# Optimization experiments

Hardware: AMD Instinct MI355X
Metric: run time of the kernel (lower is better)

Reference implementation:

```python
import jax, jax.numpy as jnp
import numpy as np

N_NODES = 100000
N_EDGES = 1600000
N_GRAPHS = 64
IN_CH, HID_CH, OUT_CH, N_CLS = 128, 128, 64, 2


def setup_inputs() -> dict:
    key = jax.random.key(0)
    ks = jax.random.split(key, 8)
    x = jax.random.normal(ks[0], (N_NODES, IN_CH), dtype=jnp.float32)
    edge_index = jax.random.randint(ks[1], (2, N_EDGES), 0, N_NODES)
    batch = jnp.sort(jax.random.randint(ks[2], (N_NODES,), 0, N_GRAPHS))
    glorot = lambda k, shp: jax.random.normal(k, shp, dtype=jnp.float32) / np.float32(np.sqrt(shp[0]))
    return {
        "x": x, "edge_index": edge_index, "batch": batch,
        "W1": glorot(ks[3], (IN_CH, HID_CH)), "b1": jnp.zeros((HID_CH,), jnp.float32),
        "W2": glorot(ks[4], (HID_CH, HID_CH)), "b2": jnp.zeros((HID_CH,), jnp.float32),
        "W3": glorot(ks[5], (HID_CH, OUT_CH)), "b3": jnp.zeros((OUT_CH,), jnp.float32),
        "Wfc": glorot(ks[6], (OUT_CH, N_CLS)), "bfc": jnp.zeros((N_CLS,), jnp.float32),
    }


def gcn_conv(x, src, dst, W, b):
    """PyG GCNConv: add self-loops, D^{-1/2} (A+I) D^{-1/2} (x W) + b."""
    n = x.shape[0]
    h = x @ W  # [N, out]
    # degree with self-loops: 1 + in-degree at dst
    deg = jnp.ones((n,), h.dtype).at[dst].add(1.0)
    dinv = jax.lax.rsqrt(deg)  # deg >= 1 always (self-loop)
    norm = dinv[src] * dinv[dst]  # [E]
    agg = jnp.zeros_like(h).at[dst].add(h[src] * norm[:, None])
    agg = agg + h * (dinv * dinv)[:, None]  # self-loop messages
    return agg + b


def global_mean_pool(x, batch, num_graphs):
    s = jax.ops.segment_sum(x, batch, num_segments=num_graphs)
    cnt = jax.ops.segment_sum(jnp.ones((x.shape[0],), x.dtype), batch, num_segments=num_graphs)
    return s / jnp.maximum(cnt, 1.0)[:, None]


def reference(x, edge_index, batch, W1, b1, W2, b2, W3, b3, Wfc, bfc):
    src, dst = edge_index[0], edge_index[1]
    h = jax.nn.relu(gcn_conv(x, src, dst, W1, b1))   # dropout p=0.0 (eval) -> identity
    h = jax.nn.relu(gcn_conv(h, src, dst, W2, b2))
    h = gcn_conv(h, src, dst, W3, b3)
    g = global_mean_pool(h, batch, N_GRAPHS)          # [G, OUT_CH]
    return g @ Wfc + bfc                              # [G, N_CLS]
```

## Files before the change

### kernel.cpp

```cpp
#include <hip/hip_runtime.h>
#include <hip/hip_bf16.h>


#define THREADS 256
#define BSHIFT 9
#define BSIZE 512

typedef __attribute__((ext_vector_type(8))) short short8;
typedef __attribute__((ext_vector_type(16))) float floatx16;

__device__ __forceinline__ unsigned f2bf(float f) {
    unsigned u = __float_as_uint(f);
    return (u + 0x7fffu + ((u >> 16) & 1u)) >> 16;
}

__device__ __forceinline__ void bf8_acc(uint4 v, float* ac) {
    ac[0] += __uint_as_float(v.x << 16);
    ac[1] += __uint_as_float(v.x & 0xffff0000u);
    ac[2] += __uint_as_float(v.y << 16);
    ac[3] += __uint_as_float(v.y & 0xffff0000u);
    ac[4] += __uint_as_float(v.z << 16);
    ac[5] += __uint_as_float(v.z & 0xffff0000u);
    ac[6] += __uint_as_float(v.w << 16);
    ac[7] += __uint_as_float(v.w & 0xffff0000u);
}


__global__ __launch_bounds__(THREADS) void bucket_count(const int* __restrict__ dst,
                                                        int* __restrict__ btotal,
                                                        int E, int nbuck) {
    __shared__ int cnt[BSIZE];
    for (int i = threadIdx.x; i < nbuck; i += THREADS) cnt[i] = 0;
    __syncthreads();
    for (int e = blockIdx.x * THREADS + threadIdx.x; e < E; e += gridDim.x * THREADS)
        atomicAdd(&cnt[dst[e] >> BSHIFT], 1);
    __syncthreads();
    for (int i = threadIdx.x; i < nbuck; i += THREADS) {
        int c = cnt[i];
        if (c) atomicAdd(&btotal[i], c);
    }
}

__global__ __launch_bounds__(512) void bucket_scan(const int* __restrict__ btotal,
                                                   int* __restrict__ bbase,
                                                   int* __restrict__ bcursor,
                                                   float* __restrict__ gsum,
                                                   float* __restrict__ zrow,
                                                   int nbuck, int E) {
    __shared__ int lds[512];
    int t = threadIdx.x;
    for (int i = t; i < 64 * 64; i += 512) gsum[i] = 0.0f;
    if (t < 64) zrow[t] = 0.0f;
    int v = (t < nbuck) ? btotal[t] : 0;
    lds[t] = v;
    __syncthreads();
    for (int off = 1; off < 512; off <<= 1) {
        int tv = (t >= off) ? lds[t - off] : 0;
        __syncthreads();
        lds[t] += tv;
        __syncthreads();
    }
    if (t < nbuck) {
        int excl = lds[t] - v;
        bbase[t] = excl;
        bcursor[t] = excl;
    }
    if (t == 0) bbase[nbuck] = E;
}

__global__ __launch_bounds__(THREADS) void bucket_scatter(const int* __restrict__ src,
                                                          const int* __restrict__ dst,
                                                          int* __restrict__ bcursor,
                                                          int* __restrict__ pairs, int E) {
    __shared__ int cnt[BSIZE];
    __shared__ int base[BSIZE];
    for (int i = threadIdx.x; i < BSIZE; i += THREADS) cnt[i] = 0;
    __syncthreads();
    int e0 = blockIdx.x * 2048;
    int myb[8], myrank[8], mypk[8];
#pragma unroll
    for (int j = 0; j < 8; ++j) {
        int e = e0 + j * THREADS + threadIdx.x;
        myb[j] = -1;
        if (e < E) {
            int d = dst[e];
            mypk[j] = (src[e] << BSHIFT) | (d & (BSIZE - 1));
            myb[j] = d >> BSHIFT;
            myrank[j] = atomicAdd(&cnt[myb[j]], 1);
        }
    }
    __syncthreads();
    for (int i = threadIdx.x; i < BSIZE; i += THREADS) {
        int c = cnt[i];
        base[i] = c ? atomicAdd(&bcursor[i], c) : 0;
    }
    __syncthreads();
#pragma unroll
    for (int j = 0; j < 8; ++j)
        if (myb[j] >= 0) pairs[(size_t)base[myb[j]] + myrank[j]] = mypk[j];
}

__global__ __launch_bounds__(512) void bucket_fill(const int* __restrict__ pairs,
                                                   const int* __restrict__ bbase,
                                                   int* __restrict__ row_start,
                                                   float* __restrict__ dinv,
                                                   int* __restrict__ esrc,
                                                   int N, int E, int nbuck) {
    __shared__ int cnt[BSIZE];
    __shared__ int scn[BSIZE];
    int b = blockIdx.x, t = threadIdx.x;
    int s = bbase[b], e = bbase[b + 1];
    cnt[t] = 0;
    __syncthreads();
    for (int i = s + t; i < e; i += 512) atomicAdd(&cnt[pairs[i] & (BSIZE - 1)], 1);
    __syncthreads();
    int v = cnt[t];
    scn[t] = v;
    __syncthreads();
    for (int off = 1; off < 512; off <<= 1) {
        int tv = (t >= off) ? scn[t - off] : 0;
        __syncthreads();
        scn[t] += tv;
        __syncthreads();
    }
    int excl = scn[t] - v;
    int g = (b << BSHIFT) + t;
    if (g < N) {
        row_start[g] = s + excl;
        dinv[g] = rsqrtf(1.0f + (float)v);
    }
    if (b == nbuck - 1 && t == 0) row_start[N] = E;
    scn[t] = excl;
    __syncthreads();
    for (int i = s + t; i < e; i += 512) {
        int p = pairs[i];
        int r = atomicAdd(&scn[p & (BSIZE - 1)], 1);
        esrc[s + r] = ((unsigned)p) >> BSHIFT;
    }
}

__device__ __forceinline__ void wt_pack(const float* W, uint4* Wtp, int C, int li) {
    int c = li >> 4, ch = li & 15;
    unsigned r[8];
#pragma unroll
    for (int j = 0; j < 8; ++j) r[j] = f2bf(W[(size_t)(ch * 8 + j) * C + c]);
    uint4 o;
    o.x = r[0] | (r[1] << 16);
    o.y = r[2] | (r[3] << 16);
    o.z = r[4] | (r[5] << 16);
    o.w = r[6] | (r[7] << 16);
    Wtp[li] = o;
}

__global__ __launch_bounds__(THREADS) void prep_wt_all(const float* __restrict__ W1,
                                                       const float* __restrict__ W2,
                                                       const float* __restrict__ W3,
                                                       uint4* __restrict__ Wt1,
                                                       uint4* __restrict__ Wt2,
                                                       uint4* __restrict__ Wt3) {
    int idx = blockIdx.x * THREADS + threadIdx.x;
    if (idx < 2048) wt_pack(W1, Wt1, 128, idx);
    else if (idx < 4096) wt_pack(W2, Wt2, 128, idx - 2048);
    else if (idx < 5120) wt_pack(W3, Wt3, 64, idx - 4096);
}

__global__ __launch_bounds__(THREADS) void prep_x(const float* __restrict__ x,
                                                  const float* __restrict__ dinv,
                                                  uint4* __restrict__ Z, int n) {
    int idx = blockIdx.x * THREADS + threadIdx.x;
    if (idx >= n * 16) return;
    int r = idx >> 4, c = idx & 15;
    float dv = dinv[r];
    const float* p = x + (size_t)r * 128 + c * 8;
    float4 a = *(const float4*)p;
    float4 b = *(const float4*)(p + 4);
    uint4 o;
    o.x = f2bf(a.x * dv) | (f2bf(a.y * dv) << 16);
    o.y = f2bf(a.z * dv) | (f2bf(a.w * dv) << 16);
    o.z = f2bf(b.x * dv) | (f2bf(b.y * dv) << 16);
    o.w = f2bf(b.z * dv) | (f2bf(b.w * dv) << 16);
    Z[idx] = o;
}

__global__ __launch_bounds__(THREADS) void fused_layer(const uint4* __restrict__ Z,
                                                       const uint4* __restrict__ Wt,
                                                       const int* __restrict__ row_start,
                                                       const int* __restrict__ esrc,
                                                       const float* __restrict__ dinv,
                                                       const float* __restrict__ bias,
                                                       const uint4* __restrict__ zrow,
                                                       uint4* __restrict__ out,
                                                       const uint4* __restrict__ WtP,
                                                       uint4* __restrict__ outP, int n) {
    __shared__ __align__(16) uint4 ldsX[64 * 16];
    int row0 = blockIdx.x * 64;
    int maxr = n - row0;
    if (maxr > 64) maxr = 64;
    int tid = threadIdx.x;
    int lane = tid & 15, grp = tid >> 4;
    const uint4* zl = zrow + lane;

    for (int round = 0; round < 4; ++round) {
        int r = round * 16 + grp;
        int node = row0 + r;
        int nd = (node < n) ? node : (n - 1);
        float ac[8] = {0, 0, 0, 0, 0, 0, 0, 0};
        bf8_acc(Z[(size_t)nd * 16 + lane], ac);
        float dv = dinv[nd];
        int s = row_start[nd], e = row_start[nd + 1];
        int i = s;
        int nmain = (e - s) >> 3;
        if (nmain > 0) {
            int s0 = esrc[i], s1 = esrc[i + 1], s2 = esrc[i + 2], s3 = esrc[i + 3];
            int s4 = esrc[i + 4], s5 = esrc[i + 5], s6 = esrc[i + 6], s7 = esrc[i + 7];
            for (int m = 0; m < nmain; ++m) {
                uint4 v0 = Z[(size_t)s0 * 16 + lane];
                uint4 v1 = Z[(size_t)s1 * 16 + lane];
                uint4 v2 = Z[(size_t)s2 * 16 + lane];
                uint4 v3 = Z[(size_t)s3 * 16 + lane];
                uint4 v4 = Z[(size_t)s4 * 16 + lane];
                uint4 v5 = Z[(size_t)s5 * 16 + lane];
                uint4 v6 = Z[(size_t)s6 * 16 + lane];
                uint4 v7 = Z[(size_t)s7 * 16 + lane];
                int ni = i + 8;
                int t0 = esrc[ni], t1 = esrc[ni + 1], t2 = esrc[ni + 2], t3 = esrc[ni + 3];
                int t4 = esrc[ni + 4], t5 = esrc[ni + 5], t6 = esrc[ni + 6], t7 = esrc[ni + 7];
                bf8_acc(v0, ac); bf8_acc(v1, ac); bf8_acc(v2, ac); bf8_acc(v3, ac);
                bf8_acc(v4, ac); bf8_acc(v5, ac); bf8_acc(v6, ac); bf8_acc(v7, ac);
                s0 = t0; s1 = t1; s2 = t2; s3 = t3;
                s4 = t4; s5 = t5; s6 = t6; s7 = t7;
                i = ni;
            }
        }
        if (i < e) {
            const uint4* p0 = (i + 0 < e) ? (Z + ((size_t)esrc[i + 0] * 16 + lane)) : zl;
            const uint4* p1 = (i + 1 < e) ? (Z + ((size_t)esrc[i + 1] * 16 + lane)) : zl;
            const uint4* p2 = (i + 2 < e) ? (Z + ((size_t)esrc[i + 2] * 16 + lane)) : zl;
            const uint4* p3 = (i + 3 < e) ? (Z + ((size_t)esrc[i + 3] * 16 + lane)) : zl;
            const uint4* p4 = (i + 4 < e) ? (Z + ((size_t)esrc[i + 4] * 16 + lane)) : zl;
            const uint4* p5 = (i + 5 < e) ? (Z + ((size_t)esrc[i + 5] * 16 + lane)) : zl;
            const uint4* p6 = (i + 6 < e) ? (Z + ((size_t)esrc[i + 6] * 16 + lane)) : zl;
            const uint4* p7 = (i + 7 < e) ? (Z + ((size_t)esrc[i + 7] * 16 + lane)) : zl;
            uint4 v0 = *p0; uint4 v1 = *p1; uint4 v2 = *p2; uint4 v3 = *p3;
            uint4 v4 = *p4; uint4 v5 = *p5; uint4 v6 = *p6; uint4 v7 = *p7;
            bf8_acc(v0, ac); bf8_acc(v1, ac); bf8_acc(v2, ac); bf8_acc(v3, ac);
            bf8_acc(v4, ac); bf8_acc(v5, ac); bf8_acc(v6, ac); bf8_acc(v7, ac);
        }
        uint4 o;
        o.x = f2bf(ac[0] * dv) | (f2bf(ac[1] * dv) << 16);
        o.y = f2bf(ac[2] * dv) | (f2bf(ac[3] * dv) << 16);
        o.z = f2bf(ac[4] * dv) | (f2bf(ac[5] * dv) << 16);
        o.w = f2bf(ac[6] * dv) | (f2bf(ac[7] * dv) << 16);
        ldsX[r * 16 + (lane ^ (r & 7))] = o;
    }
    __syncthreads();

    int l = tid & 63, wv = tid >> 6;
    int l31 = l & 31, half = l >> 5;
    int nt = wv & 1, mt0 = (wv >> 1) * 2;
    floatx16 acc[2];
#pragma unroll
    for (int t = 0; t < 2; ++t)
#pragma unroll
        for (int q = 0; q < 16; ++q) acc[t][q] = 0.0f;
    int xrow = nt * 32 + l31, xsw = xrow & 7;
#pragma unroll
    for (int kt = 0; kt < 8; ++kt) {
        int chunk = kt * 2 + half;
        short8 xf = *(const short8*)&ldsX[xrow * 16 + (chunk ^ xsw)];
#pragma unroll
        for (int t = 0; t < 2; ++t) {
            int c = (mt0 + t) * 32 + l31;
            short8 wf = *(const short8*)&Wt[c * 16 + chunk];
            acc[t] = __builtin_amdgcn_mfma_f32_32x32x16_bf16(wf, xf, acc[t], 0, 0, 0);
        }
    }
    __syncthreads();

    int node = nt * 32 + l31;
    float dv = (node < maxr) ? dinv[row0 + node] : 0.0f;
    char* outb = (char*)ldsX;
#pragma unroll
    for (int t = 0; t < 2; ++t) {
        int cb = (mt0 + t) * 32;
#pragma unroll
        for (int q = 0; q < 4; ++q) {
            float v[4];
#pragma unroll
            for (int m = 0; m < 4; ++m) {
                int ch = cb + 8 * q + 4 * half + m;
                float x_ = acc[t][q * 4 + m] + bias[ch];
                x_ = fmaxf(x_, 0.0f);
                v[m] = x_ * dv;
            }
            uint2 pk = make_uint2(f2bf(v[0]) | (f2bf(v[1]) << 16),
                                  f2bf(v[2]) | (f2bf(v[3]) << 16));
            int chunk = (cb >> 3) + q;
            *(uint2*)(outb + node * 256 + ((chunk ^ (node & 7)) * 16) + half * 8) = pk;
        }
    }
    __syncthreads();
    for (int idx = tid; idx < maxr * 16; idx += THREADS) {
        int r = idx >> 4, c = idx & 15;
        out[(size_t)(row0 + r) * 16 + c] = *(uint4*)(outb + r * 256 + ((c ^ (r & 7)) * 16));
    }

    if (outP) {
        floatx16 accp;
#pragma unroll
        for (int q = 0; q < 16; ++q) accp[q] = 0.0f;
        int mt = wv >> 1;
#pragma unroll
        for (int kt = 0; kt < 8; ++kt) {
            int chunk = kt * 2 + half;
            short8 xf = *(const short8*)&ldsX[xrow * 16 + (chunk ^ xsw)];
            int c = mt * 32 + l31;
            short8 wf = *(const short8*)&WtP[c * 16 + chunk];
            accp = __builtin_amdgcn_mfma_f32_32x32x16_bf16(wf, xf, accp, 0, 0, 0);
        }
        __syncthreads();
        int cb = mt * 32;
#pragma unroll
        for (int q = 0; q < 4; ++q) {
            uint2 pk = make_uint2(f2bf(accp[q * 4 + 0]) | (f2bf(accp[q * 4 + 1]) << 16),
                                  f2bf(accp[q * 4 + 2]) | (f2bf(accp[q * 4 + 3]) << 16));
            int chunk = (cb >> 3) + q;
            *(uint2*)(outb + node * 128 + ((chunk ^ (node & 7)) * 16) + half * 8) = pk;
        }
        __syncthreads();
        for (int idx = tid; idx < maxr * 8; idx += THREADS) {
            int r = idx >> 3, c = idx & 7;
            outP[(size_t)(row0 + r) * 8 + c] = *(uint4*)(outb + r * 128 + ((c ^ (r & 7)) * 16));
        }
    }
}

__global__ __launch_bounds__(THREADS) void agg_pool(const uint4* __restrict__ Ps,
                                                    const int* __restrict__ row_start,
                                                    const int* __restrict__ esrc,
                                                    const float* __restrict__ dinv,
                                                    const float* __restrict__ bias,
                                                    const int* __restrict__ batch,
                                                    const uint4* __restrict__ zrow,
                                                    float* __restrict__ gsum, int n) {
    __shared__ float gpart[32][65];
    __shared__ int used[32];
    int tid = threadIdx.x;
    int lane = tid & 7, grp = tid >> 3;
    int node = blockIdx.x * 32 + grp;
    if (tid < 32) used[tid] = 0;
    for (int idx = tid; idx < 2048; idx += THREADS) gpart[idx >> 6][idx & 63] = 0.0f;
    __syncthreads();
    int gmin = batch[blockIdx.x * 32];
    const uint4* zl = zrow + lane;
    if (node < n) {
        float ac[8] = {0, 0, 0, 0, 0, 0, 0, 0};
        bf8_acc(Ps[(size_t)node * 8 + lane], ac);
        float dv = dinv[node];
        int s = row_start[node], e = row_start[node + 1];
        int i = s;
        int nmain = (e - s) >> 3;
        if (nmain > 0) {
            int s0 = esrc[i], s1 = esrc[i + 1], s2 = esrc[i + 2], s3 = esrc[i + 3];
            int s4 = esrc[i + 4], s5 = esrc[i + 5], s6 = esrc[i + 6], s7 = esrc[i + 7];
            for (int m = 0; m < nmain; ++m) {
                uint4 v0 = Ps[(size_t)s0 * 8 + lane];
                uint4 v1 = Ps[(size_t)s1 * 8 + lane];
                uint4 v2 = Ps[(size_t)s2 * 8 + lane];
                uint4 v3 = Ps[(size_t)s3 * 8 + lane];
                uint4 v4 = Ps[(size_t)s4 * 8 + lane];
                uint4 v5 = Ps[(size_t)s5 * 8 + lane];
                uint4 v6 = Ps[(size_t)s6 * 8 + lane];
                uint4 v7 = Ps[(size_t)s7 * 8 + lane];
                int ni = i + 8;
                int t0 = esrc[ni], t1 = esrc[ni + 1], t2 = esrc[ni + 2], t3 = esrc[ni + 3];
                int t4 = esrc[ni + 4], t5 = esrc[ni + 5], t6 = esrc[ni + 6], t7 = esrc[ni + 7];
                bf8_acc(v0, ac); bf8_acc(v1, ac); bf8_acc(v2, ac); bf8_acc(v3, ac);
                bf8_acc(v4, ac); bf8_acc(v5, ac); bf8_acc(v6, ac); bf8_acc(v7, ac);
                s0 = t0; s1 = t1; s2 = t2; s3 = t3;
                s4 = t4; s5 = t5; s6 = t6; s7 = t7;
                i = ni;
            }
        }
        if (i < e) {
            const uint4* p0 = (i + 0 < e) ? (Ps + ((size_t)esrc[i + 0] * 8 + lane)) : zl;
            const uint4* p1 = (i + 1 < e) ? (Ps + ((size_t)esrc[i + 1] * 8 + lane)) : zl;
            const uint4* p2 = (i + 2 < e) ? (Ps + ((size_t)esrc[i + 2] * 8 + lane)) : zl;
            const uint4* p3 = (i + 3 < e) ? (Ps + ((size_t)esrc[i + 3] * 8 + lane)) : zl;
            const uint4* p4 = (i + 4 < e) ? (Ps + ((size_t)esrc[i + 4] * 8 + lane)) : zl;
            const uint4* p5 = (i + 5 < e) ? (Ps + ((size_t)esrc[i + 5] * 8 + lane)) : zl;
            const uint4* p6 = (i + 6 < e) ? (Ps + ((size_t)esrc[i + 6] * 8 + lane)) : zl;
            const uint4* p7 = (i + 7 < e) ? (Ps + ((size_t)esrc[i + 7] * 8 + lane)) : zl;
            uint4 v0 = *p0; uint4 v1 = *p1; uint4 v2 = *p2; uint4 v3 = *p3;
            uint4 v4 = *p4; uint4 v5 = *p5; uint4 v6 = *p6; uint4 v7 = *p7;
            bf8_acc(v0, ac); bf8_acc(v1, ac); bf8_acc(v2, ac); bf8_acc(v3, ac);
            bf8_acc(v4, ac); bf8_acc(v5, ac); bf8_acc(v6, ac); bf8_acc(v7, ac);
        }
        float4 b0 = ((const float4*)bias)[lane * 2];
        float4 b1 = ((const float4*)bias)[lane * 2 + 1];
        float h[8];
        h[0] = fmaf(dv, ac[0], b0.x); h[1] = fmaf(dv, ac[1], b0.y);
        h[2] = fmaf(dv, ac[2], b0.z); h[3] = fmaf(dv, ac[3], b0.w);
        h[4] = fmaf(dv, ac[4], b1.x); h[5] = fmaf(dv, ac[5], b1.y);
        h[6] = fmaf(dv, ac[6], b1.z); h[7] = fmaf(dv, ac[7], b1.w);
        int g = batch[node];
        int slot = g - gmin;
        if (slot < 32) {
            if (lane == 0) used[slot] = 1;
#pragma unroll
            for (int j = 0; j < 8; ++j) atomicAdd(&gpart[slot][lane * 8 + j], h[j]);
        } else {
#pragma unroll
            for (int j = 0; j < 8; ++j) atomicAdd(&gsum[(size_t)g * 64 + lane * 8 + j], h[j]);
        }
    }
    __syncthreads();
    for (int idx = tid; idx < 2048; idx += THREADS) {
        int s = idx >> 6, ch = idx & 63;
        if (used[s]) atomicAdd(&gsum[(size_t)(gmin + s) * 64 + ch], gpart[s][ch]);
    }
}

__device__ __forceinline__ int dev_lower_bound(const int* a, int n, int key) {
    int lo = 0, hi = n;
    while (lo < hi) {
        int mid = (lo + hi) >> 1;
        if (a[mid] < key) lo = mid + 1;
        else hi = mid;
    }
    return lo;
}

__global__ __launch_bounds__(128) void finalize_fc(const float* __restrict__ gsum,
                                                   const int* __restrict__ batch, int n,
                                                   const float* __restrict__ Wfc,
                                                   const float* __restrict__ bfc,
                                                   float* __restrict__ out) {
    __shared__ float gm[64 * 64];
    __shared__ float cnt[64];
    int t = threadIdx.x;
    if (t < 64)
        cnt[t] = (float)(dev_lower_bound(batch, n, t + 1) - dev_lower_bound(batch, n, t));
    __syncthreads();
    for (int i = t; i < 64 * 64; i += 128) gm[i] = gsum[i] / fmaxf(cnt[i >> 6], 1.0f);
    __syncthreads();
    int g = t >> 1, cls = t & 1;
    float acc = bfc[cls];
    for (int c = 0; c < 64; ++c) acc = fmaf(gm[g * 64 + c], Wfc[c * 2 + cls], acc);
    out[g * 2 + cls] = acc;
}

extern "C" void kernel_launch(void* const* d_in, const int* in_sizes, int n_in,
                              void* d_out, int out_size, void* d_ws, size_t ws_size,
                              hipStream_t stream) {
    const float* x    = (const float*)d_in[0];
    const int*   ei   = (const int*)d_in[1];
    const int*   batch= (const int*)d_in[2];
    const float* W1   = (const float*)d_in[3];
    const float* b1   = (const float*)d_in[4];
    const float* W2   = (const float*)d_in[5];
    const float* b2   = (const float*)d_in[6];
    const float* W3   = (const float*)d_in[7];
    const float* b3   = (const float*)d_in[8];
    const float* Wfc  = (const float*)d_in[9];
    const float* bfc  = (const float*)d_in[10];
    float* out = (float*)d_out;

    const int N = in_sizes[2];
    const int E = in_sizes[1] / 2;
    const int* esrc_in = ei;
    const int* edst_in = ei + E;
    const int nbuck = (N + BSIZE - 1) >> BSHIFT;

    uint4* bufA      = (uint4*)d_ws;
    uint4* bufB      = bufA + (size_t)N * 16;
    uint4* bufC      = bufB + (size_t)N * 16;
    int*   pairs     = (int*)(bufC + (size_t)N * 8);
    int*   esrc      = pairs + E;
    int*   row_start = esrc + E;
    float* dinv      = (float*)(row_start + N + 1);
    int*   btotal    = (int*)(dinv + N);
    int*   bbase     = btotal + 512;
    int*   bcursor   = bbase + 513;
    float* gsum      = (float*)(bcursor + 512);
    uint4* Wt1       = (uint4*)(gsum + 64 * 64);
    uint4* Wt2       = Wt1 + 2048;
    uint4* Wt3       = Wt2 + 2048;
    float* zrow      = (float*)(Wt3 + 1024);

    hipMemsetAsync(btotal, 0, 512 * sizeof(int), stream);
    bucket_count<<<512, THREADS, 0, stream>>>(edst_in, btotal, E, nbuck);
    bucket_scan<<<1, 512, 0, stream>>>(btotal, bbase, bcursor, gsum, zrow, nbuck, E);
    bucket_scatter<<<(E + 2047) / 2048, THREADS, 0, stream>>>(esrc_in, edst_in, bcursor, pairs, E);
    bucket_fill<<<nbuck, 512, 0, stream>>>(pairs, bbase, row_start, dinv, esrc, N, E, nbuck);
    prep_wt_all<<<20, THREADS, 0, stream>>>(W1, W2, W3, Wt1, Wt2, Wt3);
    prep_x<<<(N * 16 + THREADS - 1) / THREADS, THREADS, 0, stream>>>(x, dinv, bufA, N);

    const int GB = (N + 63) / 64;

    fused_layer<<<GB, THREADS, 0, stream>>>(bufA, Wt1, row_start, esrc, dinv, b1,
                                            (const uint4*)zrow, bufB, nullptr, nullptr, N);
    fused_layer<<<GB, THREADS, 0, stream>>>(bufB, Wt2, row_start, esrc, dinv, b2,
                                            (const uint4*)zrow, bufA, Wt3, bufC, N);
    agg_pool<<<(N + 31) / 32, THREADS, 0, stream>>>(bufC, row_start, esrc, dinv, b3, batch,
                                                    (const uint4*)zrow, gsum, N);

    finalize_fc<<<1, 128, 0, stream>>>(gsum, batch, N, Wfc, bfc, out);
}
```

Before: 416.7 us.

## Replace two-level bucket sort CSR build with global atomic counting sort

Replaces the bucketed two-pass CSR construction (bucket count, scan, scatter, per-bucket fill) with a direct per-node degree count via global atomics, a single-block 1024-thread scan over all nodes, and an atomic cursor scatter into esrc. It also merges the weight-packing and x-prep kernels into one launch. The goal is fewer kernel launches and fewer passes over edge data. In exchange it relies on global atomics contended per node, a serial single-block scan over 100k nodes, and a nondeterministic edge order within each row.

```diff
diff --git a/kernel.cpp b/kernel.cpp
--- a/kernel.cpp
+++ b/kernel.cpp
@@ -3,8 +3,6 @@
 
 
 #define THREADS 256
-#define BSHIFT 9
-#define BSIZE 512
 
 typedef __attribute__((ext_vector_type(8))) short short8;
 typedef __attribute__((ext_vector_type(16))) float floatx16;
@@ -26,116 +24,69 @@
 }
 
 
-__global__ __launch_bounds__(THREADS) void bucket_count(const int* __restrict__ dst,
-                                                        int* __restrict__ btotal,
-                                                        int E, int nbuck) {
-    __shared__ int cnt[BSIZE];
-    for (int i = threadIdx.x; i < nbuck; i += THREADS) cnt[i] = 0;
-    __syncthreads();
-    for (int e = blockIdx.x * THREADS + threadIdx.x; e < E; e += gridDim.x * THREADS)
-        atomicAdd(&cnt[dst[e] >> BSHIFT], 1);
-    __syncthreads();
-    for (int i = threadIdx.x; i < nbuck; i += THREADS) {
-        int c = cnt[i];
-        if (c) atomicAdd(&btotal[i], c);
-    }
-}
-
-__global__ __launch_bounds__(512) void bucket_scan(const int* __restrict__ btotal,
-                                                   int* __restrict__ bbase,
-                                                   int* __restrict__ bcursor,
-                                                   float* __restrict__ gsum,
-                                                   float* __restrict__ zrow,
-                                                   int nbuck, int E) {
-    __shared__ int lds[512];
+__global__ __launch_bounds__(THREADS) void deg_count(const int* __restrict__ dst,
+                                                     int* __restrict__ deg, int E) {
+#pragma unroll
+    for (int j = 0; j < 4; ++j) {
+        int e = blockIdx.x * (THREADS * 4) + j * THREADS + threadIdx.x;
+        if (e < E) atomicAdd(&deg[dst[e]], 1);
+    }
+}
+
+__global__ __launch_bounds__(1024) void scan_all(const int* __restrict__ deg,
+                                                 int* __restrict__ row_start,
+                                                 int* __restrict__ cursor,
+                                                 float* __restrict__ dinv,
+                                                 float* __restrict__ gsum,
+                                                 float* __restrict__ zrow,
+                                                 int N, int E) {
+    __shared__ int lds[1024];
     int t = threadIdx.x;
-    for (int i = t; i < 64 * 64; i += 512) gsum[i] = 0.0f;
+    int per = (N + 1023) >> 10;
+    int g0 = t * per;
+    int sum = 0;
+#pragma unroll 4
+    for (int j = 0; j < per; ++j) {
+        int g = g0 + j;
+        if (g < N) sum += deg[g];
+    }
+    lds[t] = sum;
+    __syncthreads();
+    for (int off = 1; off < 1024; off <<= 1) {
+        int v = (t >= off) ? lds[t - off] : 0;
+        __syncthreads();
+        lds[t] += v;
+        __syncthreads();
+    }
+    int run = lds[t] - sum;
+#pragma unroll 4
+    for (int j = 0; j < per; ++j) {
+        int g = g0 + j;
+        if (g < N) {
+            int d = deg[g];
+            row_start[g] = run;
+            cursor[g] = run;
+            dinv[g] = rsqrtf(1.0f + (float)d);
+            run += d;
+        }
+    }
+    if (t == 0) row_start[N] = E;
+    for (int i = t; i < 64 * 64; i += 1024) gsum[i] = 0.0f;
     if (t < 64) zrow[t] = 0.0f;
-    int v = (t < nbuck) ? btotal[t] : 0;
-    lds[t] = v;
-    __syncthreads();
-    for (int off = 1; off < 512; off <<= 1) {
-        int tv = (t >= off) ? lds[t - off] : 0;
-        __syncthreads();
-        lds[t] += tv;
-        __syncthreads();
-    }
-    if (t < nbuck) {
-        int excl = lds[t] - v;
-        bbase[t] = excl;
-        bcursor[t] = excl;
-    }
-    if (t == 0) bbase[nbuck] = E;
-}
-
-__global__ __launch_bounds__(THREADS) void bucket_scatter(const int* __restrict__ src,
-                                                          const int* __restrict__ dst,
-                                                          int* __restrict__ bcursor,
-                                                          int* __restrict__ pairs, int E) {
-    __shared__ int cnt[BSIZE];
-    __shared__ int base[BSIZE];
-    for (int i = threadIdx.x; i < BSIZE; i += THREADS) cnt[i] = 0;
-    __syncthreads();
-    int e0 = blockIdx.x * 2048;
-    int myb[8], myrank[8], mypk[8];
-#pragma unroll
-    for (int j = 0; j < 8; ++j) {
-        int e = e0 + j * THREADS + threadIdx.x;
-        myb[j] = -1;
+}
+
+__global__ __launch_bounds__(THREADS) void csr_scatter(const int* __restrict__ src,
+                                                       const int* __restrict__ dst,
+                                                       int* __restrict__ cursor,
+                                                       int* __restrict__ esrc, int E) {
+#pragma unroll
+    for (int j = 0; j < 4; ++j) {
+        int e = blockIdx.x * (THREADS * 4) + j * THREADS + threadIdx.x;
         if (e < E) {
             int d = dst[e];
-            mypk[j] = (src[e] << BSHIFT) | (d & (BSIZE - 1));
-            myb[j] = d >> BSHIFT;
-            myrank[j] = atomicAdd(&cnt[myb[j]], 1);
-        }
-    }
-    __syncthreads();
-    for (int i = threadIdx.x; i < BSIZE; i += THREADS) {
-        int c = cnt[i];
-        base[i] = c ? atomicAdd(&bcursor[i], c) : 0;
-    }
-    __syncthreads();
-#pragma unroll
-    for (int j = 0; j < 8; ++j)
-        if (myb[j] >= 0) pairs[(size_t)base[myb[j]] + myrank[j]] = mypk[j];
-}
-
-__global__ __launch_bounds__(512) void bucket_fill(const int* __restrict__ pairs,
-                                                   const int* __restrict__ bbase,
-                                                   int* __restrict__ row_start,
-                                                   float* __restrict__ dinv,
-                                                   int* __restrict__ esrc,
-                                                   int N, int E, int nbuck) {
-    __shared__ int cnt[BSIZE];
-    __shared__ int scn[BSIZE];
-    int b = blockIdx.x, t = threadIdx.x;
-    int s = bbase[b], e = bbase[b + 1];
-    cnt[t] = 0;
-    __syncthreads();
-    for (int i = s + t; i < e; i += 512) atomicAdd(&cnt[pairs[i] & (BSIZE - 1)], 1);
-    __syncthreads();
-    int v = cnt[t];
-    scn[t] = v;
-    __syncthreads();
-    for (int off = 1; off < 512; off <<= 1) {
-        int tv = (t >= off) ? scn[t - off] : 0;
-        __syncthreads();
-        scn[t] += tv;
-        __syncthreads();
-    }
-    int excl = scn[t] - v;
-    int g = (b << BSHIFT) + t;
-    if (g < N) {
-        row_start[g] = s + excl;
-        dinv[g] = rsqrtf(1.0f + (float)v);
-    }
-    if (b == nbuck - 1 && t == 0) row_start[N] = E;
-    scn[t] = excl;
-    __syncthreads();
-    for (int i = s + t; i < e; i += 512) {
-        int p = pairs[i];
-        int r = atomicAdd(&scn[p & (BSIZE - 1)], 1);
-        esrc[s + r] = ((unsigned)p) >> BSHIFT;
+            int p = atomicAdd(&cursor[d], 1);
+            esrc[p] = src[e];
+        }
     }
 }
 
@@ -152,34 +103,35 @@
     Wtp[li] = o;
 }
 
-__global__ __launch_bounds__(THREADS) void prep_wt_all(const float* __restrict__ W1,
-                                                       const float* __restrict__ W2,
-                                                       const float* __restrict__ W3,
-                                                       uint4* __restrict__ Wt1,
-                                                       uint4* __restrict__ Wt2,
-                                                       uint4* __restrict__ Wt3) {
+__global__ __launch_bounds__(THREADS) void prep_all(const float* __restrict__ x,
+                                                    const float* __restrict__ dinv,
+                                                    uint4* __restrict__ Z,
+                                                    const float* __restrict__ W1,
+                                                    const float* __restrict__ W2,
+                                                    const float* __restrict__ W3,
+                                                    uint4* __restrict__ Wt1,
+                                                    uint4* __restrict__ Wt2,
+                                                    uint4* __restrict__ Wt3, int n) {
     int idx = blockIdx.x * THREADS + threadIdx.x;
-    if (idx < 2048) wt_pack(W1, Wt1, 128, idx);
-    else if (idx < 4096) wt_pack(W2, Wt2, 128, idx - 2048);
-    else if (idx < 5120) wt_pack(W3, Wt3, 64, idx - 4096);
-}
-
-__global__ __launch_bounds__(THREADS) void prep_x(const float* __restrict__ x,
-                                                  const float* __restrict__ dinv,
-                                                  uint4* __restrict__ Z, int n) {
-    int idx = blockIdx.x * THREADS + threadIdx.x;
-    if (idx >= n * 16) return;
-    int r = idx >> 4, c = idx & 15;
-    float dv = dinv[r];
-    const float* p = x + (size_t)r * 128 + c * 8;
-    float4 a = *(const float4*)p;
-    float4 b = *(const float4*)(p + 4);
-    uint4 o;
-    o.x = f2bf(a.x * dv) | (f2bf(a.y * dv) << 16);
-    o.y = f2bf(a.z * dv) | (f2bf(a.w * dv) << 16);
-    o.z = f2bf(b.x * dv) | (f2bf(b.y * dv) << 16);
-    o.w = f2bf(b.z * dv) | (f2bf(b.w * dv) << 16);
-    Z[idx] = o;
+    int nz = n * 16;
+    if (idx < nz) {
+        int r = idx >> 4, c = idx & 15;
+        float dv = dinv[r];
+        const float* p = x + (size_t)r * 128 + c * 8;
+        float4 a = *(const float4*)p;
+        float4 b = *(const float4*)(p + 4);
+        uint4 o;
+        o.x = f2bf(a.x * dv) | (f2bf(a.y * dv) << 16);
+        o.y = f2bf(a.z * dv) | (f2bf(a.w * dv) << 16);
+        o.z = f2bf(b.x * dv) | (f2bf(b.y * dv) << 16);
+        o.w = f2bf(b.z * dv) | (f2bf(b.w * dv) << 16);
+        Z[idx] = o;
+    } else {
+        int k = idx - nz;
+        if (k < 2048) wt_pack(W1, Wt1, 128, k);
+        else if (k < 4096) wt_pack(W2, Wt2, 128, k - 2048);
+        else if (k < 5120) wt_pack(W3, Wt3, 64, k - 4096);
+    }
 }
 
 __global__ __launch_bounds__(THREADS) void fused_layer(const uint4* __restrict__ Z,
@@ -470,31 +422,28 @@
     const int E = in_sizes[1] / 2;
     const int* esrc_in = ei;
     const int* edst_in = ei + E;
-    const int nbuck = (N + BSIZE - 1) >> BSHIFT;
 
     uint4* bufA      = (uint4*)d_ws;
     uint4* bufB      = bufA + (size_t)N * 16;
     uint4* bufC      = bufB + (size_t)N * 16;
-    int*   pairs     = (int*)(bufC + (size_t)N * 8);
-    int*   esrc      = pairs + E;
-    int*   row_start = esrc + E;
+    int*   esrc      = (int*)(bufC + (size_t)N * 8);
+    int*   deg       = esrc + E;
+    int*   cursor    = deg + N;
+    int*   row_start = cursor + N;
     float* dinv      = (float*)(row_start + N + 1);
-    int*   btotal    = (int*)(dinv + N);
-    int*   bbase     = btotal + 512;
-    int*   bcursor   = bbase + 513;
-    float* gsum      = (float*)(bcursor + 512);
+    float* gsum      = (float*)(dinv + N);
     uint4* Wt1       = (uint4*)(gsum + 64 * 64);
     uint4* Wt2       = Wt1 + 2048;
     uint4* Wt3       = Wt2 + 2048;
     float* zrow      = (float*)(Wt3 + 1024);
 
-    hipMemsetAsync(btotal, 0, 512 * sizeof(int), stream);
-    bucket_count<<<512, THREADS, 0, stream>>>(edst_in, btotal, E, nbuck);
-    bucket_scan<<<1, 512, 0, stream>>>(btotal, bbase, bcursor, gsum, zrow, nbuck, E);
-    bucket_scatter<<<(E + 2047) / 2048, THREADS, 0, stream>>>(esrc_in, edst_in, bcursor, pairs, E);
-    bucket_fill<<<nbuck, 512, 0, stream>>>(pairs, bbase, row_start, dinv, esrc, N, E, nbuck);
-    prep_wt_all<<<20, THREADS, 0, stream>>>(W1, W2, W3, Wt1, Wt2, Wt3);
-    prep_x<<<(N * 16 + THREADS - 1) / THREADS, THREADS, 0, stream>>>(x, dinv, bufA, N);
+    hipMemsetAsync(deg, 0, (size_t)N * sizeof(int), stream);
+    deg_count<<<(E + THREADS * 4 - 1) / (THREADS * 4), THREADS, 0, stream>>>(edst_in, deg, E);
+    scan_all<<<1, 1024, 0, stream>>>(deg, row_start, cursor, dinv, gsum, zrow, N, E);
+    csr_scatter<<<(E + THREADS * 4 - 1) / (THREADS * 4), THREADS, 0, stream>>>(esrc_in, edst_in,
+                                                                               cursor, esrc, E);
+    prep_all<<<(N * 16 + 5120 + THREADS - 1) / THREADS, THREADS, 0, stream>>>(
+        x, dinv, bufA, W1, W2, W3, Wt1, Wt2, Wt3, N);
 
     const int GB = (N + 63) / 64;
 
```

Measured after the change: 833.1 us. +99.9%, slower.
